# Performance work log

Measured on AMD Instinct MI355X. Metric: run time of the kernel, lower is better.

## Reference

```python
import jax, jax.numpy as jnp
import numpy as np

HID = 128
EPS = 0.05
SHARP = 50.0


def _linear_init(key, fan_in, fan_out):
    # torch nn.Linear default: U(-1/sqrt(fan_in), 1/sqrt(fan_in)) for W and b
    kw, kb = jax.random.split(key)
    bound = 1.0 / np.sqrt(fan_in)
    W = jax.random.uniform(kw, (fan_in, fan_out), jnp.float32, -bound, bound)
    b = jax.random.uniform(kb, (fan_out,), jnp.float32, -bound, bound)
    return W, b


def setup_inputs() -> dict:
    key = jax.random.key(0)
    keys = jax.random.split(key, 7)
    N = 1048576
    xy = jax.random.uniform(keys[0], (N, 2), jnp.float32)  # collocation points in unit square
    U = jnp.ones((1,), jnp.float32)
    W1, b1 = _linear_init(keys[1], 2, HID)
    W2, b2 = _linear_init(keys[2], HID, HID)
    W3, b3 = _linear_init(keys[3], HID, HID)
    W4, b4 = _linear_init(keys[4], HID, HID)
    W5, b5 = _linear_init(keys[5], HID, 2)
    return {"xy": xy, "U": U, "W1": W1, "b1": b1, "W2": W2, "b2": b2,
            "W3": W3, "b3": b3, "W4": W4, "b4": b4, "W5": W5, "b5": b5}


def reference(xy, U, W1, b1, W2, b2, W3, b3, W4, b4, W5, b5):
    h = jnp.tanh(xy @ W1 + b1)
    h = jnp.tanh(h @ W2 + b2)
    h = jnp.tanh(h @ W3 + b3)
    h = jnp.tanh(h @ W4 + b4)
    out = h @ W5 + b5                      # [N, 2]
    u_hat, v_hat = out[:, 0], out[:, 1]
    x, y = xy[:, 0], xy[:, 1]
    psi = jax.nn.sigmoid(SHARP * (x - EPS)) * jax.nn.sigmoid(SHARP * (1.0 - EPS - x))
    B = x * (1.0 - x) * y * (1.0 - y)      # boundary bump
    u = U * y * psi + B * u_hat
    v = B * v_hat
    return (u, v)
```

## Files before the change

### kernel.cpp

```cpp
#include <hip/hip_runtime.h>
#include <hip/hip_bf16.h>

#define NPTS  1048576
#define GRID  512
#define NTILE 8192
#define C2    2.8853900817779268f

typedef __attribute__((ext_vector_type(8))) short  s16x8;
typedef __attribute__((ext_vector_type(4))) float  f32x4;

__device__ __forceinline__ unsigned short bf16r(float v) {
  unsigned u = __builtin_bit_cast(unsigned, v);
  return (unsigned short)((u + 0x7fffu + ((u >> 16) & 1u)) >> 16);
}
__device__ __forceinline__ unsigned pack_bf16x2(float lo, float hi) {
  __hip_bfloat162 h = __float22bfloat162_rn(float2{lo, hi});
  unsigned r;
  __builtin_memcpy(&r, &h, sizeof(r));
  return r;
}
__device__ __forceinline__ float tanh_e(float acc, float bc) {
  float e = __builtin_amdgcn_exp2f(fmaf(acc, C2, bc));
  return 1.0f - 2.0f * __builtin_amdgcn_rcpf(1.0f + e);
}
__device__ __forceinline__ float sigm_fast(float x) {
  return __builtin_amdgcn_rcpf(1.0f + __builtin_amdgcn_exp2f(x * -1.4426950408889634f));
}

__global__ void prep_kernel(const float* __restrict__ W2, const float* __restrict__ W3,
                            const float* __restrict__ W4, const float* __restrict__ W5,
                            unsigned short* __restrict__ ws)
{
  int tid = blockIdx.x * 256 + threadIdx.x;
  if (tid < 49152) {
    int l    = tid >> 14;
    int idx  = tid & 16383;
    int e    = idx & 7;
    int lane = (idx >> 3) & 63;
    int kt   = (idx >> 9) & 3;
    int nbg  = (idx >> 11) & 7;
    int k = kt * 32 + (lane >> 4) * 8 + e;
    int n = nbg * 16 + (lane & 15);
    const float* W = (l == 0) ? W2 : (l == 1) ? W3 : W4;
    ws[tid] = bf16r(W[k * 128 + n]);
  } else if (tid < 49664) {
    int idx  = tid - 49152;
    int e    = idx & 7;
    int lane = (idx >> 3) & 63;
    int kt   = idx >> 9;
    int k  = kt * 32 + (lane >> 4) * 8 + e;
    int nl = lane & 15;
    ws[tid] = (nl < 2) ? bf16r(W5[k * 2 + nl]) : (unsigned short)0;
  }
}

__global__ __launch_bounds__(256, 2)
void mlp_kernel(const float* __restrict__ xy, const float* __restrict__ Uin,
                const float* __restrict__ W1, const float* __restrict__ b1,
                const float* __restrict__ b2, const float* __restrict__ b3,
                const float* __restrict__ b4, const float* __restrict__ b5,
                const unsigned short* __restrict__ ws, float* __restrict__ out)
{
  __shared__ __align__(16) unsigned char hbuf0[32768];
  __shared__ __align__(16) unsigned char hbuf1[32768];

  const int tid  = threadIdx.x;
  const int lane = tid & 63;
  const int wid  = tid >> 6;
  const int lg   = lane >> 4;
  const int ln   = lane & 15;
  const int c0   = tid & 15;

  const float Uval = Uin[0];
  const float b50  = b5[0];
  const float b51  = b5[1];

  float bcr[3][2][4];
#pragma unroll
  for (int nb = 0; nb < 2; ++nb)
#pragma unroll
    for (int r = 0; r < 4; ++r) {
      int n = wid * 32 + nb * 16 + lg * 4 + r;
      bcr[0][nb][r] = b2[n] * C2;
      bcr[1][nb][r] = b3[n] * C2;
      bcr[2][nb][r] = b4[n] * C2;
    }

  float w1x[8], w1y[8], b1r[8];
#pragma unroll
  for (int t = 0; t < 8; ++t) {
    w1x[t] = W1[c0 * 8 + t];
    w1y[t] = W1[128 + c0 * 8 + t];
    b1r[t] = b1[c0 * 8 + t];
  }

  s16x8 Wa[3][2][4];
#pragma unroll
  for (int l = 0; l < 3; ++l)
#pragma unroll
    for (int nb = 0; nb < 2; ++nb)
#pragma unroll
      for (int kt = 0; kt < 4; ++kt)
        Wa[l][nb][kt] = *(const s16x8*)(ws + (((l * 8 + wid * 2 + nb) * 4 + kt) << 9) + lane * 8);
  s16x8 b5f[4];
#pragma unroll
  for (int kt = 0; kt < 4; ++kt)
    b5f[kt] = *(const s16x8*)(ws + 49152 + kt * 512 + lane * 8);

  const unsigned rBase = (unsigned)(ln * 256) + ((unsigned)(lg * 16) ^ ((unsigned)(ln & 7) << 4));
  unsigned wBase[2];
#pragma unroll
  for (int nb = 0; nb < 2; ++nb)
    wBase[nb] = (unsigned)(ln * 256) +
                ((unsigned)(wid * 64 + nb * 32 + lg * 8) ^ ((unsigned)(ln & 7) << 4));
  const unsigned l1Base = (unsigned)((tid >> 4) * 256) +
                          ((unsigned)(c0 * 16) ^ ((unsigned)((tid >> 4) & 7) << 4));

  for (int tile = blockIdx.x; tile < NTILE; tile += GRID) {
    const int pbase = tile << 7;

#pragma unroll
    for (int i = 0; i < 8; ++i) {
      int p = i * 16 + (tid >> 4);
      float2 v = ((const float2*)xy)[pbase + p];
      unsigned q[4];
#pragma unroll
      for (int t2 = 0; t2 < 4; ++t2) {
        float s0 = fmaf(v.x, w1x[2 * t2],     fmaf(v.y, w1y[2 * t2],     b1r[2 * t2]));
        float s1 = fmaf(v.x, w1x[2 * t2 + 1], fmaf(v.y, w1y[2 * t2 + 1], b1r[2 * t2 + 1]));
        float e0 = __builtin_amdgcn_exp2f(s0 * C2);
        float e1 = __builtin_amdgcn_exp2f(s1 * C2);
        float h0 = 1.0f - 2.0f * __builtin_amdgcn_rcpf(1.0f + e0);
        float h1 = 1.0f - 2.0f * __builtin_amdgcn_rcpf(1.0f + e1);
        q[t2] = pack_bf16x2(h0, h1);
      }
      *(uint4*)(hbuf0 + l1Base + i * 4096) = uint4{q[0], q[1], q[2], q[3]};
    }
    __syncthreads();

#pragma unroll
    for (int l = 0; l < 3; ++l) {
      const unsigned char* bufR = (l & 1) ? hbuf1 : hbuf0;
      unsigned char*       bufW = (l & 1) ? hbuf0 : hbuf1;
#pragma unroll
      for (int mt = 0; mt < 8; ++mt) {
        s16x8 B[4];
#pragma unroll
        for (int kt = 0; kt < 4; ++kt)
          B[kt] = *(const s16x8*)(bufR + rBase + mt * 4096 + kt * 64);
        f32x4 acc0 = f32x4{0.f, 0.f, 0.f, 0.f};
        f32x4 acc1 = f32x4{0.f, 0.f, 0.f, 0.f};
#pragma unroll
        for (int kt = 0; kt < 4; ++kt) {
          acc0 = __builtin_amdgcn_mfma_f32_16x16x32_bf16(Wa[l][0][kt], B[kt], acc0, 0, 0, 0);
          acc1 = __builtin_amdgcn_mfma_f32_16x16x32_bf16(Wa[l][1][kt], B[kt], acc1, 0, 0, 0);
        }
        {
          float t0 = tanh_e(acc0[0], bcr[l][0][0]);
          float t1 = tanh_e(acc0[1], bcr[l][0][1]);
          float t2 = tanh_e(acc0[2], bcr[l][0][2]);
          float t3 = tanh_e(acc0[3], bcr[l][0][3]);
          *(uint2*)(bufW + wBase[0] + mt * 4096) = uint2{pack_bf16x2(t0, t1), pack_bf16x2(t2, t3)};
        }
        {
          float t0 = tanh_e(acc1[0], bcr[l][1][0]);
          float t1 = tanh_e(acc1[1], bcr[l][1][1]);
          float t2 = tanh_e(acc1[2], bcr[l][1][2]);
          float t3 = tanh_e(acc1[3], bcr[l][1][3]);
          *(uint2*)(bufW + wBase[1] + mt * 4096) = uint2{pack_bf16x2(t0, t1), pack_bf16x2(t2, t3)};
        }
      }
      __syncthreads();
    }

    f32x4 acc5[2];
#pragma unroll
    for (int m5 = 0; m5 < 2; ++m5) acc5[m5] = f32x4{0.f, 0.f, 0.f, 0.f};
#pragma unroll
    for (int m5 = 0; m5 < 2; ++m5)
#pragma unroll
      for (int kt = 0; kt < 4; ++kt) {
        s16x8 b = *(const s16x8*)(hbuf1 + rBase + wid * 8192 + m5 * 4096 + kt * 64);
        acc5[m5] = __builtin_amdgcn_mfma_f32_16x16x32_bf16(b5f[kt], b, acc5[m5], 0, 0, 0);
      }
    if (lg == 0) {
#pragma unroll
      for (int m5 = 0; m5 < 2; ++m5) {
        int p = pbase + wid * 32 + m5 * 16 + ln;
        float uh = acc5[m5][0] + b50;
        float vh = acc5[m5][1] + b51;
        float2 v = ((const float2*)xy)[p];
        float Bm = v.x * (1.0f - v.x) * v.y * (1.0f - v.y);
        float psi = sigm_fast(50.0f * (v.x - 0.05f)) * sigm_fast(50.0f * (0.95f - v.x));
        out[p]        = fmaf(Uval * v.y, psi, Bm * uh);
        out[NPTS + p] = Bm * vh;
      }
    }
  }
}

extern "C" void kernel_launch(void* const* d_in, const int* in_sizes, int n_in,
                              void* d_out, int out_size, void* d_ws, size_t ws_size,
                              hipStream_t stream) {
  const float* xy = (const float*)d_in[0];
  const float* U  = (const float*)d_in[1];
  const float* W1 = (const float*)d_in[2];
  const float* b1 = (const float*)d_in[3];
  const float* W2 = (const float*)d_in[4];
  const float* b2 = (const float*)d_in[5];
  const float* W3 = (const float*)d_in[6];
  const float* b3 = (const float*)d_in[7];
  const float* W4 = (const float*)d_in[8];
  const float* b4 = (const float*)d_in[9];
  const float* W5 = (const float*)d_in[10];
  const float* b5 = (const float*)d_in[11];
  unsigned short* ws = (unsigned short*)d_ws;
  float* out = (float*)d_out;

  prep_kernel<<<194, 256, 0, stream>>>(W2, W3, W4, W5, ws);
  mlp_kernel<<<GRID, 256, 0, stream>>>(xy, U, W1, b1, b2, b3, b4, b5, ws, out);
}
```

Baseline: 206.5 us.

## Replace swizzled LDS activation layout with lane-contiguous fragment layout

Changes the shared-memory layout of activations so each lane's MFMA B-fragment is read from a contiguous lane*16 address per k-tile, replacing the XOR-swizzled row layout. The layer-1 writer is remapped so that each thread handles a fixed 8-column group and iterates over points. Empty asm barriers are added to keep the preloaded weight fragments resident in registers. The goal is conflict-free, simpler LDS addressing with less index arithmetic, at the cost of possible bank conflicts on the 8-byte tanh writes and higher register pressure.

New measurement: 208.1 us. About the same (+0.8%).

```diff
diff --git a/kernel.cpp b/kernel.cpp
--- a/kernel.cpp
+++ b/kernel.cpp
@@ -8,6 +8,8 @@
 
 typedef __attribute__((ext_vector_type(8))) short  s16x8;
 typedef __attribute__((ext_vector_type(4))) float  f32x4;
+
+#define KEEP(x) asm volatile("" : "+v"(x))
 
 __device__ __forceinline__ unsigned short bf16r(float v) {
   unsigned u = __builtin_bit_cast(unsigned, v);
@@ -69,6 +71,7 @@
   const int wid  = tid >> 6;
   const int lg   = lane >> 4;
   const int ln   = lane & 15;
+  const int o    = tid >> 4;
   const int c0   = tid & 15;
 
   const float Uval = Uin[0];
@@ -89,9 +92,9 @@
   float w1x[8], w1y[8], b1r[8];
 #pragma unroll
   for (int t = 0; t < 8; ++t) {
-    w1x[t] = W1[c0 * 8 + t];
-    w1y[t] = W1[128 + c0 * 8 + t];
-    b1r[t] = b1[c0 * 8 + t];
+    w1x[t] = W1[o * 8 + t];
+    w1y[t] = W1[128 + o * 8 + t];
+    b1r[t] = b1[o * 8 + t];
   }
 
   s16x8 Wa[3][2][4];
@@ -100,28 +103,28 @@
 #pragma unroll
     for (int nb = 0; nb < 2; ++nb)
 #pragma unroll
-      for (int kt = 0; kt < 4; ++kt)
+      for (int kt = 0; kt < 4; ++kt) {
         Wa[l][nb][kt] = *(const s16x8*)(ws + (((l * 8 + wid * 2 + nb) * 4 + kt) << 9) + lane * 8);
+        KEEP(Wa[l][nb][kt]);
+      }
   s16x8 b5f[4];
 #pragma unroll
-  for (int kt = 0; kt < 4; ++kt)
+  for (int kt = 0; kt < 4; ++kt) {
     b5f[kt] = *(const s16x8*)(ws + 49152 + kt * 512 + lane * 8);
-
-  const unsigned rBase = (unsigned)(ln * 256) + ((unsigned)(lg * 16) ^ ((unsigned)(ln & 7) << 4));
-  unsigned wBase[2];
-#pragma unroll
-  for (int nb = 0; nb < 2; ++nb)
-    wBase[nb] = (unsigned)(ln * 256) +
-                ((unsigned)(wid * 64 + nb * 32 + lg * 8) ^ ((unsigned)(ln & 7) << 4));
-  const unsigned l1Base = (unsigned)((tid >> 4) * 256) +
-                          ((unsigned)(c0 * 16) ^ ((unsigned)((tid >> 4) & 7) << 4));
+    KEEP(b5f[kt]);
+  }
+
+  const unsigned rBase  = (unsigned)(lane * 16);
+  const unsigned wBase0 = (unsigned)(wid * 1024 + ((lg >> 1)) * 256 + ln * 16 + (lg & 1) * 8);
+  const unsigned wBase1 = wBase0 + 512;
+  const unsigned l1Base = (unsigned)((o >> 2) * 1024 + (o & 3) * 256 + c0 * 16);
 
   for (int tile = blockIdx.x; tile < NTILE; tile += GRID) {
     const int pbase = tile << 7;
 
 #pragma unroll
     for (int i = 0; i < 8; ++i) {
-      int p = i * 16 + (tid >> 4);
+      int p = i * 16 + c0;
       float2 v = ((const float2*)xy)[pbase + p];
       unsigned q[4];
 #pragma unroll
@@ -147,7 +150,7 @@
         s16x8 B[4];
 #pragma unroll
         for (int kt = 0; kt < 4; ++kt)
-          B[kt] = *(const s16x8*)(bufR + rBase + mt * 4096 + kt * 64);
+          B[kt] = *(const s16x8*)(bufR + rBase + mt * 4096 + kt * 1024);
         f32x4 acc0 = f32x4{0.f, 0.f, 0.f, 0.f};
         f32x4 acc1 = f32x4{0.f, 0.f, 0.f, 0.f};
 #pragma unroll
@@ -160,14 +163,14 @@
           float t1 = tanh_e(acc0[1], bcr[l][0][1]);
           float t2 = tanh_e(acc0[2], bcr[l][0][2]);
           float t3 = tanh_e(acc0[3], bcr[l][0][3]);
-          *(uint2*)(bufW + wBase[0] + mt * 4096) = uint2{pack_bf16x2(t0, t1), pack_bf16x2(t2, t3)};
+          *(uint2*)(bufW + wBase0 + mt * 4096) = uint2{pack_bf16x2(t0, t1), pack_bf16x2(t2, t3)};
         }
         {
           float t0 = tanh_e(acc1[0], bcr[l][1][0]);
           float t1 = tanh_e(acc1[1], bcr[l][1][1]);
           float t2 = tanh_e(acc1[2], bcr[l][1][2]);
           float t3 = tanh_e(acc1[3], bcr[l][1][3]);
-          *(uint2*)(bufW + wBase[1] + mt * 4096) = uint2{pack_bf16x2(t0, t1), pack_bf16x2(t2, t3)};
+          *(uint2*)(bufW + wBase1 + mt * 4096) = uint2{pack_bf16x2(t0, t1), pack_bf16x2(t2, t3)};
         }
       }
       __syncthreads();
@@ -180,7 +183,7 @@
     for (int m5 = 0; m5 < 2; ++m5)
 #pragma unroll
       for (int kt = 0; kt < 4; ++kt) {
-        s16x8 b = *(const s16x8*)(hbuf1 + rBase + wid * 8192 + m5 * 4096 + kt * 64);
+        s16x8 b = *(const s16x8*)(hbuf1 + rBase + (wid * 2 + m5) * 4096 + kt * 1024);
         acc5[m5] = __builtin_amdgcn_mfma_f32_16x16x32_bf16(b5f[kt], b, acc5[m5], 0, 0, 0);
       }
     if (lg == 0) {
```
